# Performance work log

Hardware: AMD Instinct MI355X
Metric: run time of the kernel (lower is better)

The kernel has to match this reference:

```python
import jax, jax.numpy as jnp
import numpy as np
import math

CHANNEL = 512
NUM_HEAD = 8
HEAD_DIM = 64


def setup_inputs() -> dict:
    key = jax.random.key(0)
    ks = jax.random.split(key, 9)
    d = NUM_HEAD * HEAD_DIM  # 512
    s = 1.0 / math.sqrt(CHANNEL)
    return {
        "x": jax.random.normal(ks[0], (8, CHANNEL, 32, 32), dtype=jnp.float32),
        "wq": jax.random.normal(ks[1], (CHANNEL, d), dtype=jnp.float32) * s,
        "bq": jnp.zeros((d,), dtype=jnp.float32),
        "wk": jax.random.normal(ks[2], (CHANNEL, d), dtype=jnp.float32) * s,
        "bk": jnp.zeros((d,), dtype=jnp.float32),
        "wv": jax.random.normal(ks[3], (CHANNEL, d), dtype=jnp.float32) * s,
        "bv": jnp.zeros((d,), dtype=jnp.float32),
        "wo": jax.random.normal(ks[4], (d, CHANNEL), dtype=jnp.float32) * s,
        "bo": jnp.zeros((CHANNEL,), dtype=jnp.float32),
    }


def reference(x, wq, bq, wk, bk, wv, bv, wo, bo):
    B, C, H, W = x.shape
    S = H * W
    # [B, C, H, W] -> [B, S, C]
    xr = x.transpose(0, 2, 3, 1).reshape(B, S, C)
    q = (xr @ wq + bq).reshape(B, S, NUM_HEAD, HEAD_DIM)
    k = (xr @ wk + bk).reshape(B, S, NUM_HEAD, HEAD_DIM)
    v = (xr @ wv + bv).reshape(B, S, NUM_HEAD, HEAD_DIM)
    # NOTE: original scales by 1/sqrt(channel), not 1/sqrt(head_dim)
    energy = jnp.einsum('bqhd,bkhd->bhqk', q, k) / math.sqrt(C)
    attn = jax.nn.softmax(energy, axis=-1)
    out = jnp.einsum('bhqk,bkhd->bqhd', attn, v).reshape(B, S, NUM_HEAD * HEAD_DIM)
    out = out @ wo + bo  # [B, S, C]
    out = out.transpose(0, 2, 1).reshape(B, C, H, W)
    return x + out
```

## Files before the change

kernel.cpp:

```cpp
#include <hip/hip_runtime.h>
#include <hip/hip_bf16.h>

typedef __bf16 bf16_t;
typedef __attribute__((ext_vector_type(8))) __bf16 bf16x8;
typedef __attribute__((ext_vector_type(4))) __bf16 bf16x4;
typedef __attribute__((ext_vector_type(4))) float f32x4;

#define AS1 __attribute__((address_space(1)))
#define AS3 __attribute__((address_space(3)))

__device__ __forceinline__ void gload_lds16(const void* g, void* l) {
  __builtin_amdgcn_global_load_lds((const AS1 void*)g, (AS3 void*)l, 16, 0, 0);
}

__global__ void __launch_bounds__(256) prep_kernel(
    const float* __restrict__ x, const float* __restrict__ w0,
    const float* __restrict__ w1, const float* __restrict__ w2,
    const float* __restrict__ w3, bf16_t* __restrict__ xr, bf16_t* __restrict__ t0,
    bf16_t* __restrict__ t1, bf16_t* __restrict__ t2, bf16_t* __restrict__ t3) {
  __shared__ float tile[32][33];
  const int tx = threadIdx.x, ty = threadIdx.y;
  int t = blockIdx.x;
  const float* src;
  bf16_t* dst;
  int ld_src, ld_dst, r0, c0;
  if (t < 1024) {
    int z = t >> 8, rem = t & 255;
    src = (z == 0) ? w0 : (z == 1) ? w1 : (z == 2) ? w2 : w3;
    dst = (z == 0) ? t0 : (z == 1) ? t1 : (z == 2) ? t2 : t3;
    ld_src = 512; ld_dst = 512;
    r0 = (rem & 15) * 32; c0 = (rem >> 4) * 32;
  } else {
    t -= 1024;
    int b = t >> 9, rem = t & 511;
    src = x + (size_t)b * 512 * 1024;
    dst = xr + (size_t)b * 1024 * 512;
    ld_src = 1024; ld_dst = 512;
    r0 = (rem & 15) * 32; c0 = (rem >> 4) * 32;
  }
#pragma unroll
  for (int i = 0; i < 32; i += 8)
    tile[ty + i][tx] = src[(r0 + ty + i) * ld_src + c0 + tx];
  __syncthreads();
#pragma unroll
  for (int i = 0; i < 32; i += 8)
    dst[(c0 + ty + i) * ld_dst + r0 + tx] = (bf16_t)tile[tx][ty + i];
}

__device__ __forceinline__ void gemm_nt_128x128_db(const bf16_t* __restrict__ Abase,
                                                   const bf16_t* __restrict__ Bbase,
                                                   bf16_t (*As)[128 * 32],
                                                   bf16_t (*Bs)[128 * 32],
                                                   f32x4 acc[4][4]) {
  const int tid = threadIdx.x;
  const int lane = tid & 63;
  const int wid = tid >> 6;
  const int wr = wid >> 1, wc = wid & 1;
  const int lrow = lane & 15;
  const int kgrp = lane >> 4;
  const int r0 = tid >> 2;
  const int cb = (tid & 3) * 16;

#pragma unroll
  for (int j = 0; j < 2; ++j) {
    int row = j * 64 + r0;
    gload_lds16((const char*)(Abase + row * 512) + cb, (char*)As[0] + row * 64 + cb);
  }
#pragma unroll
  for (int j = 0; j < 2; ++j) {
    int row = j * 64 + r0;
    gload_lds16((const char*)(Bbase + row * 512) + cb, (char*)Bs[0] + row * 64 + cb);
  }

  for (int t = 0; t < 16; ++t) {
    const int cur = t & 1;
    if (t < 15) {
      const int kt = (t + 1) * 32;
#pragma unroll
      for (int j = 0; j < 2; ++j) {
        int row = j * 64 + r0;
        gload_lds16((const char*)(Abase + row * 512 + kt) + cb,
                    (char*)As[cur ^ 1] + row * 64 + cb);
      }
#pragma unroll
      for (int j = 0; j < 2; ++j) {
        int row = j * 64 + r0;
        gload_lds16((const char*)(Bbase + row * 512 + kt) + cb,
                    (char*)Bs[cur ^ 1] + row * 64 + cb);
      }
      asm volatile("s_waitcnt vmcnt(4)" ::: "memory");
    } else {
      asm volatile("s_waitcnt vmcnt(0)" ::: "memory");
    }
    __builtin_amdgcn_sched_barrier(0);
    __builtin_amdgcn_s_barrier();

    bf16x8 a[4], b[4];
#pragma unroll
    for (int mf = 0; mf < 4; ++mf)
      a[mf] = *(const bf16x8*)(As[cur] + (wr * 64 + mf * 16 + lrow) * 32 + kgrp * 8);
#pragma unroll
    for (int nf = 0; nf < 4; ++nf)
      b[nf] = *(const bf16x8*)(Bs[cur] + (wc * 64 + nf * 16 + lrow) * 32 + kgrp * 8);
    __builtin_amdgcn_s_setprio(1);
#pragma unroll
    for (int mf = 0; mf < 4; ++mf)
#pragma unroll
      for (int nf = 0; nf < 4; ++nf)
        acc[mf][nf] = __builtin_amdgcn_mfma_f32_16x16x32_bf16(a[mf], b[nf], acc[mf][nf], 0, 0, 0);
    __builtin_amdgcn_s_setprio(0);
    asm volatile("s_waitcnt lgkmcnt(0)" ::: "memory");
    __builtin_amdgcn_sched_barrier(0);
    __builtin_amdgcn_s_barrier();
  }
}

__global__ void __launch_bounds__(256) gemm_qkv_kernel(
    const bf16_t* __restrict__ xr, const bf16_t* __restrict__ wqT,
    const bf16_t* __restrict__ wkT, const bf16_t* __restrict__ wvT,
    const float* __restrict__ bq, const float* __restrict__ bk,
    const float* __restrict__ bv, bf16_t* __restrict__ qo, bf16_t* __restrict__ ko,
    bf16_t* __restrict__ vto) {
  __shared__ bf16_t As[2][128 * 32];
  __shared__ bf16_t Bs[2][128 * 32];
  const int bn = blockIdx.x, bm = blockIdx.y, z = blockIdx.z;
  const bf16_t* wT = (z == 0) ? wqT : (z == 1) ? wkT : wvT;
  const float* bias = (z == 0) ? bq : (z == 1) ? bk : bv;
  f32x4 acc[4][4] = {};
  gemm_nt_128x128_db(xr + bm * 128 * 512, wT + bn * 128 * 512, As, Bs, acc);
  const int lane = threadIdx.x & 63, wid = threadIdx.x >> 6;
  const int lrow = lane & 15, kgrp = lane >> 4;
  const int wr = wid >> 1, wc = wid & 1;
  const int row0 = bm * 128 + wr * 64;
  const int col0 = bn * 128 + wc * 64;
  const float qscale = 0.044194173824159216f * 1.4426950408889634f;
  if (z == 2) {
#pragma unroll
    for (int mf = 0; mf < 4; ++mf)
#pragma unroll
      for (int nf = 0; nf < 4; ++nf) {
        int n = col0 + nf * 16 + lrow;
        int h = n >> 6, d = n & 63;
        float bb = bias[n];
        int m0 = row0 + mf * 16 + kgrp * 4;
        int b = m0 >> 10, s = m0 & 1023;
        bf16x4 pk;
#pragma unroll
        for (int r = 0; r < 4; ++r) pk[r] = (bf16_t)(acc[mf][nf][r] + bb);
        *(bf16x4*)(vto + (((size_t)(b * 8 + h) * 64 + d) * 1024 + s)) = pk;
      }
  } else {
    bf16_t* out = (z == 0) ? qo : ko;
    const float sc = (z == 0) ? qscale : 1.0f;
#pragma unroll
    for (int mf = 0; mf < 4; ++mf)
#pragma unroll
      for (int nf = 0; nf < 4; ++nf) {
        int n = col0 + nf * 16 + lrow;
        int h = n >> 6, d = n & 63;
        float bb = bias[n];
#pragma unroll
        for (int r = 0; r < 4; ++r) {
          int m = row0 + mf * 16 + kgrp * 4 + r;
          int b = m >> 10, s = m & 1023;
          out[((b * 8 + h) * 1024 + s) * 64 + d] = (bf16_t)((acc[mf][nf][r] + bb) * sc);
        }
      }
  }
}

__global__ void __launch_bounds__(256, 4) attn_kernel(const bf16_t* __restrict__ q,
                                                      const bf16_t* __restrict__ k,
                                                      const bf16_t* __restrict__ vt,
                                                      bf16_t* __restrict__ attn_out) {
  __shared__ char Ks[2][8192];
  __shared__ char Vs[2][8192];
  __shared__ char Ps[4][2048];
  const int tid = threadIdx.x;
  const int lane = tid & 63, wid = tid >> 6;
  const int lrow = lane & 15, kgrp = lane >> 4;
  const int bh = blockIdx.y, qb = blockIdx.x;
  const int b = bh >> 3, h = bh & 7;

  const char* khb = (const char*)(k + (size_t)bh * 1024 * 64);
  const char* vthb = (const char*)(vt + (size_t)bh * 64 * 1024);
  const bf16_t* qh = q + (size_t)bh * 1024 * 64;

  const int qrow = qb * 64 + wid * 16 + lrow;
  const bf16x8 qa0 = *(const bf16x8*)(qh + qrow * 64 + kgrp * 8);
  const bf16x8 qa1 = *(const bf16x8*)(qh + qrow * 64 + 32 + kgrp * 8);

  char* Pw = Ps[wid];
  const int srow = tid >> 3;
  const int sc2 = tid & 7;

  float l_part = 0.f;
  f32x4 o[4] = {};

#pragma unroll
  for (int j = 0; j < 2; ++j) {
    int row = j * 32 + srow;
    gload_lds16(khb + row * 128 + ((sc2 ^ (row & 7)) * 16), Ks[0] + j * 4096 + tid * 16);
  }
#pragma unroll
  for (int j = 0; j < 2; ++j) {
    int row = j * 32 + srow;
    gload_lds16(vthb + row * 2048 + ((sc2 ^ (row & 7)) * 16), Vs[0] + j * 4096 + tid * 16);
  }

  for (int t = 0; t < 16; ++t) {
    const int cur = t & 1;
    if (t < 15) {
      const char* kg = khb + (t + 1) * (64 * 128);
      const char* vg = vthb + (t + 1) * 128;
#pragma unroll
      for (int j = 0; j < 2; ++j) {
        int row = j * 32 + srow;
        gload_lds16(kg + row * 128 + ((sc2 ^ (row & 7)) * 16),
                    Ks[cur ^ 1] + j * 4096 + tid * 16);
      }
#pragma unroll
      for (int j = 0; j < 2; ++j) {
        int row = j * 32 + srow;
        gload_lds16(vg + row * 2048 + ((sc2 ^ (row & 7)) * 16),
                    Vs[cur ^ 1] + j * 4096 + tid * 16);
      }
      asm volatile("s_waitcnt vmcnt(4)" ::: "memory");
    } else {
      asm volatile("s_waitcnt vmcnt(0)" ::: "memory");
    }
    __builtin_amdgcn_sched_barrier(0);
    __builtin_amdgcn_s_barrier();

    const char* Kc = Ks[cur];
    const char* Vc = Vs[cur];

    f32x4 sa[4] = {};
    __builtin_amdgcn_s_setprio(1);
#pragma unroll
    for (int c = 0; c < 4; ++c) {
      int krow = c * 16 + lrow;
      bf16x8 k0 = *(const bf16x8*)(Kc + krow * 128 + ((kgrp ^ (krow & 7)) * 16));
      bf16x8 k1 = *(const bf16x8*)(Kc + krow * 128 + (((4 + kgrp) ^ (krow & 7)) * 16));
      sa[c] = __builtin_amdgcn_mfma_f32_16x16x32_bf16(k0, qa0, sa[c], 0, 0, 0);
      sa[c] = __builtin_amdgcn_mfma_f32_16x16x32_bf16(k1, qa1, sa[c], 0, 0, 0);
    }
    __builtin_amdgcn_s_setprio(0);

    float rs = 0.f;
#pragma unroll
    for (int c = 0; c < 4; ++c)
#pragma unroll
      for (int r = 0; r < 4; ++r) {
        float p = exp2f(sa[c][r]);
        sa[c][r] = p;
        rs += p;
      }
    l_part += rs;

#pragma unroll
    for (int c = 0; c < 4; ++c) {
      bf16x4 pk;
#pragma unroll
      for (int r = 0; r < 4; ++r) pk[r] = (bf16_t)sa[c][r];
      int chunk = (c * 2 + (kgrp >> 1)) ^ (lrow & 7);
      *(bf16x4*)(Pw + lrow * 128 + chunk * 16 + (kgrp & 1) * 8) = pk;
    }

    __builtin_amdgcn_s_setprio(1);
#pragma unroll
    for (int kk = 0; kk < 2; ++kk) {
      int pchunk = (kk * 4 + kgrp) ^ (lrow & 7);
      bf16x8 pa = *(const bf16x8*)(Pw + lrow * 128 + pchunk * 16);
#pragma unroll
      for (int nfo = 0; nfo < 4; ++nfo) {
        int vrow = nfo * 16 + lrow;
        int vchunk = (kk * 4 + kgrp) ^ (vrow & 7);
        bf16x8 vb = *(const bf16x8*)(Vc + vrow * 128 + vchunk * 16);
        o[nfo] = __builtin_amdgcn_mfma_f32_16x16x32_bf16(pa, vb, o[nfo], 0, 0, 0);
      }
    }
    __builtin_amdgcn_s_setprio(0);
    __builtin_amdgcn_s_barrier();
  }

  l_part += __shfl_xor(l_part, 16, 64);
  l_part += __shfl_xor(l_part, 32, 64);
  float inv[4];
#pragma unroll
  for (int r = 0; r < 4; ++r) inv[r] = 1.0f / __shfl(l_part, kgrp * 4 + r, 64);
#pragma unroll
  for (int r = 0; r < 4; ++r) {
    int s = qb * 64 + wid * 16 + kgrp * 4 + r;
#pragma unroll
    for (int nfo = 0; nfo < 4; ++nfo) {
      int d = nfo * 16 + lrow;
      attn_out[((b * 1024 + s) * 8 + h) * 64 + d] = (bf16_t)(o[nfo][r] * inv[r]);
    }
  }
}

__global__ void __launch_bounds__(256) gemm_out_kernel(const bf16_t* __restrict__ woT,
                                                       const bf16_t* __restrict__ attn,
                                                       const float* __restrict__ x,
                                                       const float* __restrict__ bo,
                                                       float* __restrict__ out) {
  __shared__ bf16_t As[2][128 * 32];
  __shared__ bf16_t Bs[2][128 * 32];
  const int bn = blockIdx.x, bm = blockIdx.y;
  f32x4 acc[4][4] = {};
  gemm_nt_128x128_db(woT + bm * 128 * 512, attn + bn * 128 * 512, As, Bs, acc);
  const int lane = threadIdx.x & 63, wid = threadIdx.x >> 6;
  const int wr = wid >> 1, wc = wid & 1;
  const int c0 = bm * 128 + wr * 64;
  const int s0g = bn * 128 + wc * 64;
#pragma unroll
  for (int mf = 0; mf < 4; ++mf)
#pragma unroll
    for (int r = 0; r < 4; ++r) {
      int c = c0 + mf * 16 + (lane >> 4) * 4 + r;
      float bias = bo[c];
#pragma unroll
      for (int nf = 0; nf < 4; ++nf) {
        int n = s0g + nf * 16 + (lane & 15);
        int b = n >> 10, s = n & 1023;
        int idx = (b * 512 + c) * 1024 + s;
        out[idx] = x[idx] + acc[mf][nf][r] + bias;
      }
    }
}

extern "C" void kernel_launch(void* const* d_in, const int* in_sizes, int n_in,
                              void* d_out, int out_size, void* d_ws, size_t ws_size,
                              hipStream_t stream) {
  const float* x  = (const float*)d_in[0];
  const float* wq = (const float*)d_in[1];
  const float* bq = (const float*)d_in[2];
  const float* wk = (const float*)d_in[3];
  const float* bk = (const float*)d_in[4];
  const float* wv = (const float*)d_in[5];
  const float* bv = (const float*)d_in[6];
  const float* wo = (const float*)d_in[7];
  const float* bo = (const float*)d_in[8];
  float* out = (float*)d_out;

  char* ws = (char*)d_ws;
  const size_t SZ_XR = (size_t)8192 * 512 * 2;
  const size_t SZ_W  = (size_t)512 * 512 * 2;
  const size_t SZ_T  = (size_t)8 * 8 * 1024 * 64 * 2;
  bf16_t* xr   = (bf16_t*)(ws);
  bf16_t* wqT  = (bf16_t*)(ws + SZ_XR);
  bf16_t* wkT  = (bf16_t*)(ws + SZ_XR + SZ_W);
  bf16_t* wvT  = (bf16_t*)(ws + SZ_XR + 2 * SZ_W);
  bf16_t* woT  = (bf16_t*)(ws + SZ_XR + 3 * SZ_W);
  bf16_t* qd   = (bf16_t*)(ws + SZ_XR + 4 * SZ_W);
  bf16_t* kd   = (bf16_t*)(ws + SZ_XR + 4 * SZ_W + SZ_T);
  bf16_t* vtd  = (bf16_t*)(ws + SZ_XR + 4 * SZ_W + 2 * SZ_T);
  bf16_t* attn = (bf16_t*)(ws);

  prep_kernel<<<dim3(5120), dim3(32, 8), 0, stream>>>(x, wq, wk, wv, wo, xr, wqT, wkT,
                                                      wvT, woT);
  gemm_qkv_kernel<<<dim3(4, 64, 3), 256, 0, stream>>>(xr, wqT, wkT, wvT, bq, bk, bv,
                                                      qd, kd, vtd);
  attn_kernel<<<dim3(16, 64), 256, 0, stream>>>(qd, kd, vtd, attn);
  gemm_out_kernel<<<dim3(64, 4), 256, 0, stream>>>(woT, attn, x, bo, out);
}
```

Measured before the change: 98.63 us.

## Double query rows per attention wave to reuse K/V tiles across two fragments

```diff
diff --git a/kernel.cpp b/kernel.cpp
--- a/kernel.cpp
+++ b/kernel.cpp
@@ -169,33 +169,38 @@
   }
 }
 
-__global__ void __launch_bounds__(256, 4) attn_kernel(const bf16_t* __restrict__ q,
+__global__ void __launch_bounds__(256, 2) attn_kernel(const bf16_t* __restrict__ q,
                                                       const bf16_t* __restrict__ k,
                                                       const bf16_t* __restrict__ vt,
                                                       bf16_t* __restrict__ attn_out) {
   __shared__ char Ks[2][8192];
   __shared__ char Vs[2][8192];
-  __shared__ char Ps[4][2048];
+  __shared__ char Ps[4][4096];
   const int tid = threadIdx.x;
   const int lane = tid & 63, wid = tid >> 6;
   const int lrow = lane & 15, kgrp = lane >> 4;
-  const int bh = blockIdx.y, qb = blockIdx.x;
+  const int bh = blockIdx.x, qb = blockIdx.y;
   const int b = bh >> 3, h = bh & 7;
 
   const char* khb = (const char*)(k + (size_t)bh * 1024 * 64);
   const char* vthb = (const char*)(vt + (size_t)bh * 64 * 1024);
   const bf16_t* qh = q + (size_t)bh * 1024 * 64;
 
-  const int qrow = qb * 64 + wid * 16 + lrow;
-  const bf16x8 qa0 = *(const bf16x8*)(qh + qrow * 64 + kgrp * 8);
-  const bf16x8 qa1 = *(const bf16x8*)(qh + qrow * 64 + 32 + kgrp * 8);
+  const int qbase = qb * 128 + wid * 32;
+  bf16x8 qa[2][2];
+#pragma unroll
+  for (int qf = 0; qf < 2; ++qf) {
+    int qrow = qbase + qf * 16 + lrow;
+    qa[qf][0] = *(const bf16x8*)(qh + qrow * 64 + kgrp * 8);
+    qa[qf][1] = *(const bf16x8*)(qh + qrow * 64 + 32 + kgrp * 8);
+  }
 
   char* Pw = Ps[wid];
   const int srow = tid >> 3;
   const int sc2 = tid & 7;
 
-  float l_part = 0.f;
-  f32x4 o[4] = {};
+  float l_part[2] = {0.f, 0.f};
+  f32x4 o[2][4] = {};
 
 #pragma unroll
   for (int j = 0; j < 2; ++j) {
@@ -235,69 +240,81 @@
     const char* Kc = Ks[cur];
     const char* Vc = Vs[cur];
 
-    f32x4 sa[4] = {};
+    f32x4 sa[2][4] = {};
     __builtin_amdgcn_s_setprio(1);
 #pragma unroll
     for (int c = 0; c < 4; ++c) {
       int krow = c * 16 + lrow;
       bf16x8 k0 = *(const bf16x8*)(Kc + krow * 128 + ((kgrp ^ (krow & 7)) * 16));
       bf16x8 k1 = *(const bf16x8*)(Kc + krow * 128 + (((4 + kgrp) ^ (krow & 7)) * 16));
-      sa[c] = __builtin_amdgcn_mfma_f32_16x16x32_bf16(k0, qa0, sa[c], 0, 0, 0);
-      sa[c] = __builtin_amdgcn_mfma_f32_16x16x32_bf16(k1, qa1, sa[c], 0, 0, 0);
+#pragma unroll
+      for (int qf = 0; qf < 2; ++qf) {
+        sa[qf][c] = __builtin_amdgcn_mfma_f32_16x16x32_bf16(k0, qa[qf][0], sa[qf][c], 0, 0, 0);
+        sa[qf][c] = __builtin_amdgcn_mfma_f32_16x16x32_bf16(k1, qa[qf][1], sa[qf][c], 0, 0, 0);
+      }
     }
     __builtin_amdgcn_s_setprio(0);
 
-    float rs = 0.f;
-#pragma unroll
-    for (int c = 0; c < 4; ++c)
-#pragma unroll
-      for (int r = 0; r < 4; ++r) {
-        float p = exp2f(sa[c][r]);
-        sa[c][r] = p;
-        rs += p;
-      }
-    l_part += rs;
-
-#pragma unroll
-    for (int c = 0; c < 4; ++c) {
-      bf16x4 pk;
-#pragma unroll
-      for (int r = 0; r < 4; ++r) pk[r] = (bf16_t)sa[c][r];
-      int chunk = (c * 2 + (kgrp >> 1)) ^ (lrow & 7);
-      *(bf16x4*)(Pw + lrow * 128 + chunk * 16 + (kgrp & 1) * 8) = pk;
+#pragma unroll
+    for (int qf = 0; qf < 2; ++qf) {
+      int prow = qf * 16 + lrow;
+      float rs = 0.f;
+#pragma unroll
+      for (int c = 0; c < 4; ++c) {
+        bf16x4 pk;
+#pragma unroll
+        for (int r = 0; r < 4; ++r) {
+          float p = exp2f(sa[qf][c][r]);
+          rs += p;
+          pk[r] = (bf16_t)p;
+        }
+        int chunk = (c * 2 + (kgrp >> 1)) ^ (prow & 7);
+        *(bf16x4*)(Pw + prow * 128 + chunk * 16 + (kgrp & 1) * 8) = pk;
+      }
+      l_part[qf] += rs;
     }
 
     __builtin_amdgcn_s_setprio(1);
 #pragma unroll
     for (int kk = 0; kk < 2; ++kk) {
-      int pchunk = (kk * 4 + kgrp) ^ (lrow & 7);
-      bf16x8 pa = *(const bf16x8*)(Pw + lrow * 128 + pchunk * 16);
+      bf16x8 pa[2];
+#pragma unroll
+      for (int qf = 0; qf < 2; ++qf) {
+        int prow = qf * 16 + lrow;
+        int pchunk = (kk * 4 + kgrp) ^ (prow & 7);
+        pa[qf] = *(const bf16x8*)(Pw + prow * 128 + pchunk * 16);
+      }
 #pragma unroll
       for (int nfo = 0; nfo < 4; ++nfo) {
         int vrow = nfo * 16 + lrow;
         int vchunk = (kk * 4 + kgrp) ^ (vrow & 7);
         bf16x8 vb = *(const bf16x8*)(Vc + vrow * 128 + vchunk * 16);
-        o[nfo] = __builtin_amdgcn_mfma_f32_16x16x32_bf16(pa, vb, o[nfo], 0, 0, 0);
+#pragma unroll
+        for (int qf = 0; qf < 2; ++qf)
+          o[qf][nfo] = __builtin_amdgcn_mfma_f32_16x16x32_bf16(pa[qf], vb, o[qf][nfo], 0, 0, 0);
       }
     }
     __builtin_amdgcn_s_setprio(0);
     __builtin_amdgcn_s_barrier();
   }
 
-  l_part += __shfl_xor(l_part, 16, 64);
-  l_part += __shfl_xor(l_part, 32, 64);
-  float inv[4];
-#pragma unroll
-  for (int r = 0; r < 4; ++r) inv[r] = 1.0f / __shfl(l_part, kgrp * 4 + r, 64);
-#pragma unroll
-  for (int r = 0; r < 4; ++r) {
-    int s = qb * 64 + wid * 16 + kgrp * 4 + r;
-#pragma unroll
-    for (int nfo = 0; nfo < 4; ++nfo) {
-      int d = nfo * 16 + lrow;
-      attn_out[((b * 1024 + s) * 8 + h) * 64 + d] = (bf16_t)(o[nfo][r] * inv[r]);
-    }
-  }
+#pragma unroll
+  for (int qf = 0; qf < 2; ++qf) {
+    l_part[qf] += __shfl_xor(l_part[qf], 16, 64);
+    l_part[qf] += __shfl_xor(l_part[qf], 32, 64);
+  }
+#pragma unroll
+  for (int qf = 0; qf < 2; ++qf)
+#pragma unroll
+    for (int r = 0; r < 4; ++r) {
+      float inv = 1.0f / __shfl(l_part[qf], kgrp * 4 + r, 64);
+      int s = qbase + qf * 16 + kgrp * 4 + r;
+#pragma unroll
+      for (int nfo = 0; nfo < 4; ++nfo) {
+        int d = nfo * 16 + lrow;
+        attn_out[((b * 1024 + s) * 8 + h) * 64 + d] = (bf16_t)(o[qf][nfo][r] * inv);
+      }
+    }
 }
 
 __global__ void __launch_bounds__(256) gemm_out_kernel(const bf16_t* __restrict__ woT,
@@ -362,6 +379,6 @@
                                                       wvT, woT);
   gemm_qkv_kernel<<<dim3(4, 64, 3), 256, 0, stream>>>(xr, wqT, wkT, wvT, bq, bk, bv,
                                                       qd, kd, vtd);
-  attn_kernel<<<dim3(16, 64), 256, 0, stream>>>(qd, kd, vtd, attn);
+  attn_kernel<<<dim3(64, 8), 256, 0, stream>>>(qd, kd, vtd, attn);
   gemm_out_kernel<<<dim3(64, 4), 256, 0, stream>>>(woT, attn, x, bo, out);
 }
```

Result: no change. 98.54 us (-0.1%).
